# Optimization experiments

Measured on AMD Instinct MI355X. Metric: run time of the kernel, lower is better.

The kernel has to match this reference:

```python
import jax, jax.numpy as jnp
import numpy as np

G = 8  # order of C8 rotation group

def expand_circulant(w):
    # w: [out_fields, in_fields, G] free params of a C8 regular->regular 1x1 conv.
    # Full weight: W[of*G+go, if*G+gi] = w[of, if, (go-gi) mod G]
    g = jnp.arange(G)
    idx = (g[:, None] - g[None, :]) % G            # [go, gi]
    Wf = w[:, :, idx]                              # [of, if, go, gi]
    Wf = jnp.transpose(Wf, (0, 2, 1, 3))           # [of, go, if, gi]
    return Wf.reshape(w.shape[0] * G, w.shape[1] * G)

def eq_proj(x2, w, b):
    # x2: [B, in_fields*G]; equivariant 1x1 conv = GEMM with circulant-expanded weight
    Wf = expand_circulant(w)                       # [out_fields*G, in_fields*G]
    bf = jnp.repeat(b, G)                          # per-field bias, shared across group dim
    return x2 @ Wf.T + bf

def setup_inputs() -> dict:
    key = jax.random.key(0)
    ks = jax.random.split(key, 12)
    B, d_model, n_head, d_k, d_v = 8192, 128, 8, 64, 64
    C = d_model * G                                # 1024
    s_in = 0.02
    inp = {
        'q': jax.random.normal(ks[0], (B, C, 1, 1), jnp.float32),
        'k': jax.random.normal(ks[1], (B, C, 1, 1), jnp.float32),
        'v': jax.random.normal(ks[2], (B, C, 1, 1), jnp.float32),
        'w_q': jax.random.normal(ks[3], (n_head * d_k, d_model, G), jnp.float32) * s_in,
        'b_q': jnp.zeros((n_head * d_k,), jnp.float32),
        'w_k': jax.random.normal(ks[4], (n_head * d_k, d_model, G), jnp.float32) * s_in,
        'b_k': jnp.zeros((n_head * d_k,), jnp.float32),
        'w_v': jax.random.normal(ks[5], (n_head * d_v, d_model, G), jnp.float32) * s_in,
        'b_v': jnp.zeros((n_head * d_v,), jnp.float32),
        'w_fc': jax.random.normal(ks[6], (d_model, n_head * d_v, G), jnp.float32) * s_in,
        'b_fc': jnp.zeros((d_model,), jnp.float32),
    }
    return inp

def reference(q, k, v, w_q, b_q, w_k, b_k, w_v, b_v, w_fc, b_fc):
    B, C = q.shape[0], q.shape[1]
    n_head, d_k = 8, 64
    d_v = 64
    temp = jnp.asarray(d_k ** 0.5, q.dtype)
    residual = q                                   # [B, C, 1, 1]
    q2 = q.reshape(B, C)
    k2 = k.reshape(B, C)
    v2 = v.reshape(B, C)
    # equivariant 1x1 conv projections -> [B, n_head*d_k*G]
    qp = eq_proj(q2, w_q, b_q).reshape(B, G, n_head, d_k).transpose(0, 2, 1, 3)  # [B,H,G,dk]
    kp = eq_proj(k2, w_k, b_k).reshape(B, G, n_head, d_k).transpose(0, 2, 1, 3)
    vp = eq_proj(v2, w_v, b_v).reshape(B, G, n_head, d_v).transpose(0, 2, 1, 3)
    # scaled dot-product attention over the G=8 group/orientation positions
    attn = jax.nn.softmax(jnp.einsum('bhqd,bhkd->bhqk', qp / temp, kp), axis=-1)  # [B,H,G,G]
    out = jnp.einsum('bhqk,bhkd->bhqd', attn, vp)  # [B,H,G,dv]
    # transpose(1,2) then flatten, exactly as torch .view(sz_b, -1, 1, 1)
    out = out.transpose(0, 2, 1, 3).reshape(B, G * n_head * d_v)
    out = eq_proj(out, w_fc, b_fc)                 # [B, d_model*G]
    out = out.reshape(B, C, 1, 1) + residual
    return out, attn
```

## Files before the change

### kernel.cpp

```cpp
#include <hip/hip_runtime.h>
#include <hip/hip_bf16.h>

typedef unsigned short u16;
typedef unsigned int u32;
typedef __bf16 bf16x8_t __attribute__((ext_vector_type(8)));
typedef float f32x4_t __attribute__((ext_vector_type(4)));

#define BK 64

__device__ __forceinline__ float b2f(u16 v) {
  return __uint_as_float(((u32)v) << 16);
}
__device__ __forceinline__ u16 f2b(float f) {
  __hip_bfloat16 h = __float2bfloat16(f);
  return *reinterpret_cast<u16*>(&h);
}
__device__ __forceinline__ float blo(u32 u) { return __uint_as_float(u << 16); }
__device__ __forceinline__ float bhi(u32 u) { return __uint_as_float(u & 0xffff0000u); }

__device__ __forceinline__ void async_lds16(const u16* g, u16* l) {
  __builtin_amdgcn_global_load_lds(
      (__attribute__((address_space(1))) void*)g,
      (__attribute__((address_space(3))) void*)l, 16, 0, 0);
}

__device__ __forceinline__ void expand8(const float* __restrict__ w,
                                        u16* __restrict__ dst, int I,
                                        int kshift, int gid) {
  const int n = gid >> kshift;
  const int kc = (gid & ((1 << kshift) - 1)) * 8;
  const int K = 8 << kshift;
  const float* wp = w + (size_t)((n >> 3) * I + (kc >> 3)) * 8;
  float4 w0 = *(const float4*)wp;
  float4 w1 = *(const float4*)(wp + 4);
  float w8[8] = {w0.x, w0.y, w0.z, w0.w, w1.x, w1.y, w1.z, w1.w};
  u16 t[8];
  const int r = (n - kc) & 7;
#pragma unroll
  for (int j = 0; j < 8; ++j) t[j] = f2b(w8[(r - j) & 7]);
  *(uint4*)(dst + (size_t)n * K + kc) = *(const uint4*)t;
}

__global__ __launch_bounds__(256) void expand_all(
    const float* __restrict__ w_q, const float* __restrict__ w_k,
    const float* __restrict__ w_v, const float* __restrict__ w_fc,
    u16* __restrict__ Wq, u16* __restrict__ Wk, u16* __restrict__ Wv,
    u16* __restrict__ Wfc) {
  const int e = blockIdx.x;
  const int plane = e >> 11;
  const int gid = (e & 2047) * 256 + threadIdx.x;
  if (plane == 0) expand8(w_q, Wq, 128, 7, gid);
  else if (plane == 1) expand8(w_k, Wk, 128, 7, gid);
  else if (plane == 2) expand8(w_v, Wv, 128, 7, gid);
  else expand8(w_fc, Wfc, 512, 9, gid);
}

template <int TN, bool HAS_RES, bool OUT_F32, bool A_F32>
__device__ __forceinline__ void gemm_core(
    const void* __restrict__ Xv, const u16* __restrict__ W,
    const float* __restrict__ bias, const float* __restrict__ res,
    void* __restrict__ Yv, int M, int N, int K, int bid) {
  __shared__ __align__(16) u16 As[128 * BK];
  __shared__ __align__(16) u16 Bs[TN * BK];
  const int tid = threadIdx.x;

  const int grid_m = M >> 7, grid_n = N / TN;
  const int nb = grid_m * grid_n;
  int pid = (bid & 7) * (nb >> 3) + (bid >> 3);
  const int nig = 8 * grid_n;
  const int group_id = pid / nig;
  const int first_m = group_id * 8;
  const int gsz = min(8, grid_m - first_m);
  const int mt = first_m + (pid % gsz);
  const int nt = (pid % nig) / gsz;
  const int m0 = mt << 7, n0 = nt * TN;

  const int lane = tid & 63;
  const int wave = tid >> 6;
  const int wm = (wave >> 1) * 64;
  const int wn = (wave & 1) * (TN / 2);
  const int l16 = lane & 15;
  const int quad = lane >> 4;
  constexpr int NJ = TN >> 5;

  f32x4_t acc[4][NJ] = {};

  const int row0 = tid >> 3;
  const int kgl = ((tid & 7) ^ (row0 & 7)) * 8;

  for (int k0 = 0; k0 < K; k0 += BK) {
#pragma unroll
    for (int it = 0; it < TN / 32; ++it)
      async_lds16(W + (size_t)(n0 + row0 + it * 32) * K + (k0 + kgl),
                  &Bs[(tid + it * 256) * 8]);
    if (A_F32) {
      const float* Xf = (const float*)Xv;
      float4 fa[4], fb[4];
#pragma unroll
      for (int it = 0; it < 4; ++it) {
        const float* p = Xf + (size_t)(m0 + row0 + it * 32) * K + (k0 + kgl);
        fa[it] = *(const float4*)p;
        fb[it] = *(const float4*)(p + 4);
      }
#pragma unroll
      for (int it = 0; it < 4; ++it) {
        u16 t[8] = {f2b(fa[it].x), f2b(fa[it].y), f2b(fa[it].z), f2b(fa[it].w),
                    f2b(fb[it].x), f2b(fb[it].y), f2b(fb[it].z), f2b(fb[it].w)};
        *(uint4*)&As[(tid + it * 256) * 8] = *(const uint4*)t;
      }
    } else {
      const u16* Xb = (const u16*)Xv;
#pragma unroll
      for (int it = 0; it < 4; ++it)
        async_lds16(Xb + (size_t)(m0 + row0 + it * 32) * K + (k0 + kgl),
                    &As[(tid + it * 256) * 8]);
    }
    __syncthreads();
#pragma unroll
    for (int half = 0; half < 2; ++half) {
      bf16x8_t af[4], bfr[NJ];
#pragma unroll
      for (int i = 0; i < 4; ++i)
        af[i] = *(const bf16x8_t*)&As[(wm + i * 16 + l16) * BK +
                                      (((quad + half * 4) ^ (l16 & 7)) * 8)];
#pragma unroll
      for (int j = 0; j < NJ; ++j)
        bfr[j] = *(const bf16x8_t*)&Bs[(wn + j * 16 + l16) * BK +
                                       (((quad + half * 4) ^ (l16 & 7)) * 8)];
#pragma unroll
      for (int i = 0; i < 4; ++i)
#pragma unroll
        for (int j = 0; j < NJ; ++j)
          acc[i][j] =
              __builtin_amdgcn_mfma_f32_16x16x32_bf16(af[i], bfr[j], acc[i][j], 0, 0, 0);
    }
    __syncthreads();
  }

#pragma unroll
  for (int j = 0; j < NJ; ++j) {
    const int col = n0 + wn + j * 16 + l16;
    const float bv = bias[col >> 3];
#pragma unroll
    for (int i = 0; i < 4; ++i) {
#pragma unroll
      for (int r = 0; r < 4; ++r) {
        const int rw = m0 + wm + i * 16 + quad * 4 + r;
        float vv = acc[i][j][r] + bv;
        if (HAS_RES) vv += res[(size_t)rw * N + col];
        if (OUT_F32)
          ((float*)Yv)[(size_t)rw * N + col] = vv;
        else
          ((u16*)Yv)[(size_t)rw * N + col] = f2b(vv);
      }
    }
  }
}

__global__ __launch_bounds__(256) void gemm_qkv(
    const float* __restrict__ X0, const float* __restrict__ X1,
    const float* __restrict__ X2, const u16* __restrict__ W0,
    const u16* __restrict__ W1, const u16* __restrict__ W2,
    const float* __restrict__ b0, const float* __restrict__ b1,
    const float* __restrict__ b2, u16* __restrict__ Y0, u16* __restrict__ Y1,
    u16* __restrict__ Y2, int M, int N, int K) {
  const int z = blockIdx.y;
  const float* X = (z == 0) ? X0 : (z == 1) ? X1 : X2;
  const u16* W = (z == 0) ? W0 : (z == 1) ? W1 : W2;
  const float* bb = (z == 0) ? b0 : (z == 1) ? b1 : b2;
  u16* Y = (z == 0) ? Y0 : (z == 1) ? Y1 : Y2;
  gemm_core<128, false, false, true>(X, W, bb, nullptr, Y, M, N, K, blockIdx.x);
}

__global__ __launch_bounds__(256) void gemm_fc(
    const u16* __restrict__ X, const u16* __restrict__ W,
    const float* __restrict__ bias, const float* __restrict__ res,
    float* __restrict__ Y, int M, int N, int K) {
  gemm_core<64, true, true, false>(X, W, bias, res, Y, M, N, K, blockIdx.x);
}

__global__ __launch_bounds__(256) void attn_kernel(
    const u16* __restrict__ qp, const u16* __restrict__ kp,
    const u16* __restrict__ vp, float* __restrict__ probs,
    u16* __restrict__ o, int iters) {
  __shared__ __align__(16) u16 Qs[4][8 * 72];
  __shared__ __align__(16) u16 Ks[4][8 * 72];
  __shared__ __align__(16) float Ps[4][64];
  const int tid = threadIdx.x;
  const int wave = tid >> 6;
  const int lane = tid & 63;
  const int r = lane >> 3, c = lane & 7;
  const int ls = r * 72 + c * 8;
  const int qg = r;
  const int kg = c;

  auto pairof = [&](int it) { return (it * gridDim.x + blockIdx.x) * 4 + wave; };
  auto gaddr = [&](int it) {
    const int pr = pairof(it);
    return (size_t)(pr >> 3) * 4096 + (size_t)r * 512 + (pr & 7) * 64 + c * 8;
  };

  uint4 qr = *(const uint4*)(qp + gaddr(0));
  uint4 kr = *(const uint4*)(kp + gaddr(0));

  for (int it = 0; it < iters; ++it) {
    *(uint4*)&Qs[wave][ls] = qr;
    *(uint4*)&Ks[wave][ls] = kr;
    const int pair = pairof(it);
    const int b = pair >> 3;
    const int h = pair & 7;
    float vcf[8];
#pragma unroll
    for (int k2 = 0; k2 < 8; ++k2)
      vcf[k2] = b2f(vp[(size_t)b * 4096 + (size_t)k2 * 512 + h * 64 + lane]);
    if (it + 1 < iters) {
      qr = *(const uint4*)(qp + gaddr(it + 1));
      kr = *(const uint4*)(kp + gaddr(it + 1));
    }
    float s = 0.f;
#pragma unroll
    for (int d8 = 0; d8 < 8; ++d8) {
      uint4 qa = *(const uint4*)&Qs[wave][qg * 72 + d8 * 8];
      uint4 ka = *(const uint4*)&Ks[wave][kg * 72 + d8 * 8];
      s += blo(qa.x) * blo(ka.x) + bhi(qa.x) * bhi(ka.x);
      s += blo(qa.y) * blo(ka.y) + bhi(qa.y) * bhi(ka.y);
      s += blo(qa.z) * blo(ka.z) + bhi(qa.z) * bhi(ka.z);
      s += blo(qa.w) * blo(ka.w) + bhi(qa.w) * bhi(ka.w);
    }
    s *= 0.125f;
    float mx = s;
    mx = fmaxf(mx, __shfl_xor(mx, 1));
    mx = fmaxf(mx, __shfl_xor(mx, 2));
    mx = fmaxf(mx, __shfl_xor(mx, 4));
    float e = __expf(s - mx);
    float sum = e;
    sum += __shfl_xor(sum, 1);
    sum += __shfl_xor(sum, 2);
    sum += __shfl_xor(sum, 4);
    const float p = e / sum;
    probs[(size_t)pair * 64 + lane] = p;
    Ps[wave][lane] = p;
#pragma unroll
    for (int q2 = 0; q2 < 8; ++q2) {
      float4 p0 = *(const float4*)&Ps[wave][q2 * 8];
      float4 p1 = *(const float4*)&Ps[wave][q2 * 8 + 4];
      float acc = p0.x * vcf[0] + p0.y * vcf[1] + p0.z * vcf[2] + p0.w * vcf[3] +
                  p1.x * vcf[4] + p1.y * vcf[5] + p1.z * vcf[6] + p1.w * vcf[7];
      o[(size_t)b * 4096 + q2 * 512 + h * 64 + lane] = f2b(acc);
    }
  }
}

extern "C" void kernel_launch(void* const* d_in, const int* in_sizes, int n_in,
                              void* d_out, int out_size, void* d_ws, size_t ws_size,
                              hipStream_t stream) {
  const float* q = (const float*)d_in[0];
  const float* k = (const float*)d_in[1];
  const float* v = (const float*)d_in[2];
  const float* w_q = (const float*)d_in[3];
  const float* b_q = (const float*)d_in[4];
  const float* w_k = (const float*)d_in[5];
  const float* b_k = (const float*)d_in[6];
  const float* w_v = (const float*)d_in[7];
  const float* b_v = (const float*)d_in[8];
  const float* w_fc = (const float*)d_in[9];
  const float* b_fc = (const float*)d_in[10];

  const int B = in_sizes[0] / 1024;
  float* out = (float*)d_out;
  float* probs = out + (size_t)B * 1024;

  u16* Wq = (u16*)d_ws;
  u16* Wk = Wq + (size_t)4096 * 1024;
  u16* Wv = Wk + (size_t)4096 * 1024;
  u16* Wfc = Wv + (size_t)4096 * 1024;
  u16* scratch = Wfc + (size_t)4096 * 1024;
  const size_t wbytes = (size_t)4 * 4096 * 1024 * sizeof(u16);

  const size_t per_row = (size_t)(4 * 4096) * sizeof(u16);
  int chunkB = 128;
  for (int c = B; c >= 128; c >>= 1) {
    if (wbytes + (size_t)c * per_row <= ws_size) { chunkB = c; break; }
  }

  u16* qp = scratch;
  u16* kp = qp + (size_t)chunkB * 4096;
  u16* vp = kp + (size_t)chunkB * 4096;
  u16* ao = vp + (size_t)chunkB * 4096;

  expand_all<<<8192, 256, 0, stream>>>(w_q, w_k, w_v, w_fc, Wq, Wk, Wv, Wfc);

  for (int cs = 0; cs < B; cs += chunkB) {
    const int nb_p = (chunkB / 128) * (4096 / 128);
    gemm_qkv<<<dim3(nb_p, 3), 256, 0, stream>>>(
        q + (size_t)cs * 1024, k + (size_t)cs * 1024, v + (size_t)cs * 1024,
        Wq, Wk, Wv, b_q, b_k, b_v, qp, kp, vp, chunkB, 4096, 1024);
    const int ablocks = (chunkB >= 1024) ? 2048 : chunkB * 2;
    const int aiters = (chunkB * 8) / (ablocks * 4);
    attn_kernel<<<ablocks, 256, 0, stream>>>(qp, kp, vp,
                                             probs + (size_t)cs * 512, ao, aiters);
    const int nb_fc = (chunkB / 128) * (1024 / 64);
    gemm_fc<<<nb_fc, 256, 0, stream>>>(ao, Wfc, b_fc, q + (size_t)cs * 1024,
                                       out + (size_t)cs * 1024, chunkB, 1024,
                                       4096);
  }
}
```

Before: 601.2 us.

## Pre-convert q/k/v to bf16 in expand kernel; use 128-wide tiles for fc GEMM

The fp32-to-bf16 conversion of the q, k and v inputs moves out of the QKV GEMM's inner loop and into the weight-expansion kernel, which now writes bf16 copies into the workspace. The QKV GEMM can then load its A tiles with async global-to-LDS copies, as it already does for B. The fc GEMM also switches from a 64-wide to a 128-wide N tile, halving its block count and raising reuse per block. The cost is an extra pass that writes and re-reads 3*B*1024 bf16 values, a larger fixed workspace that can shrink chunkB, and fewer blocks in the fc launch.

```diff
diff --git a/kernel.cpp b/kernel.cpp
--- a/kernel.cpp
+++ b/kernel.cpp
@@ -41,23 +41,44 @@
   *(uint4*)(dst + (size_t)n * K + kc) = *(const uint4*)t;
 }
 
+__device__ __forceinline__ void cvt8(const float* __restrict__ src,
+                                     u16* __restrict__ dst, int gid) {
+  const float* p = src + (size_t)gid * 8;
+  float4 a = *(const float4*)p;
+  float4 b = *(const float4*)(p + 4);
+  u16 t[8] = {f2b(a.x), f2b(a.y), f2b(a.z), f2b(a.w),
+              f2b(b.x), f2b(b.y), f2b(b.z), f2b(b.w)};
+  *(uint4*)(dst + (size_t)gid * 8) = *(const uint4*)t;
+}
+
 __global__ __launch_bounds__(256) void expand_all(
     const float* __restrict__ w_q, const float* __restrict__ w_k,
     const float* __restrict__ w_v, const float* __restrict__ w_fc,
-    u16* __restrict__ Wq, u16* __restrict__ Wk, u16* __restrict__ Wv,
-    u16* __restrict__ Wfc) {
+    const float* __restrict__ q, const float* __restrict__ k,
+    const float* __restrict__ v, u16* __restrict__ Wq, u16* __restrict__ Wk,
+    u16* __restrict__ Wv, u16* __restrict__ Wfc, u16* __restrict__ qb,
+    u16* __restrict__ kb, u16* __restrict__ vb, int cblocks) {
   const int e = blockIdx.x;
-  const int plane = e >> 11;
-  const int gid = (e & 2047) * 256 + threadIdx.x;
-  if (plane == 0) expand8(w_q, Wq, 128, 7, gid);
-  else if (plane == 1) expand8(w_k, Wk, 128, 7, gid);
-  else if (plane == 2) expand8(w_v, Wv, 128, 7, gid);
-  else expand8(w_fc, Wfc, 512, 9, gid);
-}
-
-template <int TN, bool HAS_RES, bool OUT_F32, bool A_F32>
+  if (e < 8192) {
+    const int plane = e >> 11;
+    const int gid = (e & 2047) * 256 + threadIdx.x;
+    if (plane == 0) expand8(w_q, Wq, 128, 7, gid);
+    else if (plane == 1) expand8(w_k, Wk, 128, 7, gid);
+    else if (plane == 2) expand8(w_v, Wv, 128, 7, gid);
+    else expand8(w_fc, Wfc, 512, 9, gid);
+  } else {
+    const int ce = e - 8192;
+    const int plane = ce / cblocks;
+    const int gid = (ce - plane * cblocks) * 256 + threadIdx.x;
+    if (plane == 0) cvt8(q, qb, gid);
+    else if (plane == 1) cvt8(k, kb, gid);
+    else cvt8(v, vb, gid);
+  }
+}
+
+template <int TN, bool HAS_RES, bool OUT_F32>
 __device__ __forceinline__ void gemm_core(
-    const void* __restrict__ Xv, const u16* __restrict__ W,
+    const u16* __restrict__ Xb, const u16* __restrict__ W,
     const float* __restrict__ bias, const float* __restrict__ res,
     void* __restrict__ Yv, int M, int N, int K, int bid) {
   __shared__ __align__(16) u16 As[128 * BK];
@@ -93,28 +114,10 @@
     for (int it = 0; it < TN / 32; ++it)
       async_lds16(W + (size_t)(n0 + row0 + it * 32) * K + (k0 + kgl),
                   &Bs[(tid + it * 256) * 8]);
-    if (A_F32) {
-      const float* Xf = (const float*)Xv;
-      float4 fa[4], fb[4];
-#pragma unroll
-      for (int it = 0; it < 4; ++it) {
-        const float* p = Xf + (size_t)(m0 + row0 + it * 32) * K + (k0 + kgl);
-        fa[it] = *(const float4*)p;
-        fb[it] = *(const float4*)(p + 4);
-      }
-#pragma unroll
-      for (int it = 0; it < 4; ++it) {
-        u16 t[8] = {f2b(fa[it].x), f2b(fa[it].y), f2b(fa[it].z), f2b(fa[it].w),
-                    f2b(fb[it].x), f2b(fb[it].y), f2b(fb[it].z), f2b(fb[it].w)};
-        *(uint4*)&As[(tid + it * 256) * 8] = *(const uint4*)t;
-      }
-    } else {
-      const u16* Xb = (const u16*)Xv;
-#pragma unroll
-      for (int it = 0; it < 4; ++it)
-        async_lds16(Xb + (size_t)(m0 + row0 + it * 32) * K + (k0 + kgl),
-                    &As[(tid + it * 256) * 8]);
-    }
+#pragma unroll
+    for (int it = 0; it < 4; ++it)
+      async_lds16(Xb + (size_t)(m0 + row0 + it * 32) * K + (k0 + kgl),
+                  &As[(tid + it * 256) * 8]);
     __syncthreads();
 #pragma unroll
     for (int half = 0; half < 2; ++half) {
@@ -158,25 +161,25 @@
 }
 
 __global__ __launch_bounds__(256) void gemm_qkv(
-    const float* __restrict__ X0, const float* __restrict__ X1,
-    const float* __restrict__ X2, const u16* __restrict__ W0,
+    const u16* __restrict__ X0, const u16* __restrict__ X1,
+    const u16* __restrict__ X2, const u16* __restrict__ W0,
     const u16* __restrict__ W1, const u16* __restrict__ W2,
     const float* __restrict__ b0, const float* __restrict__ b1,
     const float* __restrict__ b2, u16* __restrict__ Y0, u16* __restrict__ Y1,
     u16* __restrict__ Y2, int M, int N, int K) {
   const int z = blockIdx.y;
-  const float* X = (z == 0) ? X0 : (z == 1) ? X1 : X2;
+  const u16* X = (z == 0) ? X0 : (z == 1) ? X1 : X2;
   const u16* W = (z == 0) ? W0 : (z == 1) ? W1 : W2;
   const float* bb = (z == 0) ? b0 : (z == 1) ? b1 : b2;
   u16* Y = (z == 0) ? Y0 : (z == 1) ? Y1 : Y2;
-  gemm_core<128, false, false, true>(X, W, bb, nullptr, Y, M, N, K, blockIdx.x);
+  gemm_core<128, false, false>(X, W, bb, nullptr, Y, M, N, K, blockIdx.x);
 }
 
 __global__ __launch_bounds__(256) void gemm_fc(
     const u16* __restrict__ X, const u16* __restrict__ W,
     const float* __restrict__ bias, const float* __restrict__ res,
     float* __restrict__ Y, int M, int N, int K) {
-  gemm_core<64, true, true, false>(X, W, bias, res, Y, M, N, K, blockIdx.x);
+  gemm_core<128, true, true>(X, W, bias, res, Y, M, N, K, blockIdx.x);
 }
 
 __global__ __launch_bounds__(256) void attn_kernel(
@@ -274,13 +277,17 @@
   u16* Wk = Wq + (size_t)4096 * 1024;
   u16* Wv = Wk + (size_t)4096 * 1024;
   u16* Wfc = Wv + (size_t)4096 * 1024;
-  u16* scratch = Wfc + (size_t)4096 * 1024;
-  const size_t wbytes = (size_t)4 * 4096 * 1024 * sizeof(u16);
+  u16* qb = Wfc + (size_t)4096 * 1024;
+  u16* kb = qb + (size_t)B * 1024;
+  u16* vb = kb + (size_t)B * 1024;
+  u16* scratch = vb + (size_t)B * 1024;
+  const size_t fixed_bytes =
+      ((size_t)4 * 4096 * 1024 + (size_t)3 * B * 1024) * sizeof(u16);
 
   const size_t per_row = (size_t)(4 * 4096) * sizeof(u16);
   int chunkB = 128;
   for (int c = B; c >= 128; c >>= 1) {
-    if (wbytes + (size_t)c * per_row <= ws_size) { chunkB = c; break; }
+    if (fixed_bytes + (size_t)c * per_row <= ws_size) { chunkB = c; break; }
   }
 
   u16* qp = scratch;
@@ -288,18 +295,20 @@
   u16* vp = kp + (size_t)chunkB * 4096;
   u16* ao = vp + (size_t)chunkB * 4096;
 
-  expand_all<<<8192, 256, 0, stream>>>(w_q, w_k, w_v, w_fc, Wq, Wk, Wv, Wfc);
+  const int cblocks = B / 2;
+  expand_all<<<8192 + 3 * cblocks, 256, 0, stream>>>(
+      w_q, w_k, w_v, w_fc, q, k, v, Wq, Wk, Wv, Wfc, qb, kb, vb, cblocks);
 
   for (int cs = 0; cs < B; cs += chunkB) {
     const int nb_p = (chunkB / 128) * (4096 / 128);
     gemm_qkv<<<dim3(nb_p, 3), 256, 0, stream>>>(
-        q + (size_t)cs * 1024, k + (size_t)cs * 1024, v + (size_t)cs * 1024,
+        qb + (size_t)cs * 1024, kb + (size_t)cs * 1024, vb + (size_t)cs * 1024,
         Wq, Wk, Wv, b_q, b_k, b_v, qp, kp, vp, chunkB, 4096, 1024);
     const int ablocks = (chunkB >= 1024) ? 2048 : chunkB * 2;
     const int aiters = (chunkB * 8) / (ablocks * 4);
     attn_kernel<<<ablocks, 256, 0, stream>>>(qp, kp, vp,
                                              probs + (size_t)cs * 512, ao, aiters);
-    const int nb_fc = (chunkB / 128) * (1024 / 64);
+    const int nb_fc = (chunkB / 128) * (1024 / 128);
     gemm_fc<<<nb_fc, 256, 0, stream>>>(ao, Wfc, b_fc, q + (size_t)cs * 1024,
                                        out + (size_t)cs * 1024, chunkB, 1024,
                                        4096);
```

Measured after the change: 677.4 us. +12.7%, slower.
